# Performance work log

Measured on AMD Instinct MI355X. Metric: run time of the kernel, lower is better.

The kernel has to match this reference:

```python
import jax, jax.numpy as jnp
import numpy as np

EPS = 1e-5


def layer_norm(x, g, b):
    mu = jnp.mean(x, axis=-1, keepdims=True)
    var = jnp.mean((x - mu) ** 2, axis=-1, keepdims=True)
    return (x - mu) * jax.lax.rsqrt(var + EPS) * g + b


def rel_enc_shift(arr):
    # Transformer-XL shift trick: [b,n,l,m] -> shifted [b,n,l,m]
    b, n, l, m = arr.shape
    arr = jnp.concatenate([arr, jnp.zeros((b, n, l, 1), arr.dtype)], axis=-1)
    arr = arr.reshape(b, n, -1)
    arr = arr[:, :, l - 1:-1].reshape(b, n, l, m)
    return arr


def setup_inputs() -> dict:
    key = jax.random.key(0)
    B, S, M, D, H = 2, 1024, 1024, 1024, 16
    F = S + M
    ks = jax.random.split(key, 16)
    sc = 0.02
    inp = {
        "inputs": jax.random.normal(ks[0], (B, S, D), jnp.float32),
        "mem": jax.random.normal(ks[1], (B, M, D), jnp.float32),
        "rel_enc": jax.random.normal(ks[2], (F, D), jnp.float32),
        # causal mask with memory: query i may attend keys j <= i + M; 1 = masked
        "mask": (jnp.arange(F)[None, :] > (jnp.arange(S)[:, None] + M)).astype(jnp.float32)[None, None],
        "ln1_g": jnp.ones((D,), jnp.float32), "ln1_b": jnp.zeros((D,), jnp.float32),
        "wq": jax.random.normal(ks[3], (D, D), jnp.float32) * sc,
        "wke": jax.random.normal(ks[4], (D, D), jnp.float32) * sc,
        "wkr": jax.random.normal(ks[5], (D, D), jnp.float32) * sc,
        "wv": jax.random.normal(ks[6], (D, D), jnp.float32) * sc,
        "wf": jax.random.normal(ks[7], (D, D), jnp.float32) * sc,
        "u_param": jax.random.normal(ks[8], (1, 1, H, D // H), jnp.float32) * 0.05,
        "v_param": jax.random.normal(ks[9], (1, 1, H, D // H), jnp.float32) * 0.05,
        "ln2_g": jnp.ones((D,), jnp.float32), "ln2_b": jnp.zeros((D,), jnp.float32),
        "w1": jax.random.normal(ks[10], (D, D), jnp.float32) * sc,
        "b1": jnp.zeros((D,), jnp.float32),
        "w2": jax.random.normal(ks[11], (D, D), jnp.float32) * sc,
        "b2": jnp.zeros((D,), jnp.float32),
        "wg1": jax.random.normal(ks[12], (D, D), jnp.float32) * sc,
        "bg1": jnp.zeros((D,), jnp.float32),
        "wg2": jax.random.normal(ks[13], (D, D), jnp.float32) * sc,
        "bg2": jnp.zeros((D,), jnp.float32),
    }
    return inp


def _block(inputs, mem, mask, rel_enc, ln1_g, ln1_b, wq, wke, wkr, wv, wf,
           u_param, v_param, ln2_g, ln2_b, w1, b1, w2, b2, wg1, bg1, wg2, bg2):
    B, S, D = inputs.shape
    H = u_param.shape[2]
    dh = D // H
    x_tilde = jnp.concatenate([jax.lax.stop_gradient(mem), inputs], axis=1)
    F = x_tilde.shape[1]
    x_tilde = layer_norm(x_tilde, ln1_g, ln1_b)
    x = x_tilde[:, -S:, :]
    q = (x @ wq).reshape(B, S, H, dh)
    k = (x_tilde @ wke).reshape(B, F, H, dh)
    v = (x_tilde @ wv).reshape(B, F, H, dh)
    A_C = jnp.einsum('bsnd,bfnd->bnsf', q + u_param, k)
    Q = (rel_enc @ wkr).reshape(F, H, dh)
    B_D = rel_enc_shift(jnp.einsum('bsnd,fnd->bnsf', q + v_param, Q))
    score = (A_C + B_D) / jnp.sqrt(jnp.float32(D)) + mask * -1e10
    attn = jax.nn.softmax(score, axis=-1)
    attention_loss = jnp.mean(jnp.max(attn, axis=(-1, -2)))
    ao = jnp.einsum('bnsf,bfnd->bsnd', attn, v).reshape(B, S, D)
    rmha_out = jax.nn.gelu(ao @ wf, approximate=False)
    # gating 1 (output gating): x + sigmoid(Wx+b)*y
    g1 = inputs + jax.nn.sigmoid(inputs @ wg1 + bg1) * rmha_out
    h = layer_norm(g1, ln2_g, ln2_b)
    h = jax.nn.gelu(h @ w1 + b1, approximate=False)
    h = jax.nn.gelu(h @ w2 + b2, approximate=False)
    out = g1 + jax.nn.sigmoid(g1 @ wg2 + bg2) * h
    return out, attn, attention_loss


def reference(inputs, mem, mask, rel_enc, ln1_g, ln1_b, wq, wke, wkr, wv, wf,
              u_param, v_param, ln2_g, ln2_b, w1, b1, w2, b2, wg1, bg1, wg2, bg2):
    return _block(inputs, mem, mask, rel_enc, ln1_g, ln1_b, wq, wke, wkr, wv, wf,
                  u_param, v_param, ln2_g, ln2_b, w1, b1, w2, b2, wg1, bg1, wg2, bg2)
```

## Files before the change

### kernel.cpp

```cpp
#include <hip/hip_runtime.h>
#include <hip/hip_bf16.h>


typedef __attribute__((ext_vector_type(8))) short bf16x8;
typedef __attribute__((ext_vector_type(4))) float f32x4;

#define MFMA16(a, b, c) __builtin_amdgcn_mfma_f32_16x16x32_bf16((a), (b), (c), 0, 0, 0)

__device__ __forceinline__ unsigned short f2bf(float f) {
  union { __hip_bfloat16 h; unsigned short u; } cv;
  cv.h = __float2bfloat16(f);
  return cv.u;
}

__device__ __forceinline__ float bf2f(unsigned short u) {
  return __uint_as_float((unsigned)u << 16);
}

__device__ __forceinline__ float gelu_f(float x) {
  return 0.5f * x * (1.f + erff(x * 0.70710678118654752f));
}

struct W9 { const float* p[9]; };

__global__ __launch_bounds__(256) void k_init(
    const float* __restrict__ inputs, const float* __restrict__ mem,
    const float* __restrict__ rel_enc, const float* __restrict__ g1n,
    const float* __restrict__ b1n, W9 wp,
    unsigned short* __restrict__ xt, unsigned short* __restrict__ inb,
    unsigned short* __restrict__ reb, unsigned short* __restrict__ wT,
    float* __restrict__ amax) {
  int bid = blockIdx.x, tid = threadIdx.x;
  if (bid == 0 && tid < 32) amax[tid] = 0.f;
  if (bid < 4096) {
    __shared__ float red[8];
    int b = bid >> 11, fi = bid & 2047;
    const float* src = (fi < 1024)
        ? (mem + ((size_t)(b * 1024 + fi)) * 1024)
        : (inputs + ((size_t)(b * 1024 + fi - 1024)) * 1024);
    float4 x = ((const float4*)src)[tid];
    float s = x.x + x.y + x.z + x.w;
    float ss = x.x * x.x + x.y * x.y + x.z * x.z + x.w * x.w;
#pragma unroll
    for (int m = 32; m > 0; m >>= 1) {
      s += __shfl_down(s, m, 64);
      ss += __shfl_down(ss, m, 64);
    }
    int w = tid >> 6;
    if ((tid & 63) == 0) { red[w] = s; red[4 + w] = ss; }
    __syncthreads();
    s = red[0] + red[1] + red[2] + red[3];
    ss = red[4] + red[5] + red[6] + red[7];
    float mu = s * (1.f / 1024.f);
    float inv = rsqrtf(ss * (1.f / 1024.f) - mu * mu + 1e-5f);
    float4 g = ((const float4*)g1n)[tid];
    float4 bb = ((const float4*)b1n)[tid];
    ushort4 o;
    o.x = f2bf((x.x - mu) * inv * g.x + bb.x);
    o.y = f2bf((x.y - mu) * inv * g.y + bb.y);
    o.z = f2bf((x.z - mu) * inv * g.z + bb.z);
    o.w = f2bf((x.w - mu) * inv * g.w + bb.w);
    ((ushort4*)(xt + (size_t)bid * 1024))[tid] = o;
    if (fi >= 1024) {
      ushort4 r4;
      r4.x = f2bf(x.x); r4.y = f2bf(x.y); r4.z = f2bf(x.z); r4.w = f2bf(x.w);
      ((ushort4*)(inb + ((size_t)(b * 1024 + fi - 1024)) * 1024))[tid] = r4;
    }
  } else if (bid < 6144) {
    int r = bid - 4096;
    float4 x = ((const float4*)(rel_enc + (size_t)r * 1024))[tid];
    ushort4 o;
    o.x = f2bf(x.x); o.y = f2bf(x.y); o.z = f2bf(x.z); o.w = f2bf(x.w);
    ((ushort4*)(reb + (size_t)r * 1024))[tid] = o;
  } else {
    __shared__ float tl[64][65];
    int idx = bid - 6144;
    int m = idx >> 8;
    int t = idx & 255;
    int k0 = (t >> 4) << 6, n0 = (t & 15) << 6;
    const float* srcw = wp.p[m];
    int kr = tid >> 4, nc = (tid & 15) << 2;
#pragma unroll
    for (int i = 0; i < 4; ++i) {
      int krow = i * 16 + kr;
      float4 v = *(const float4*)(srcw + (size_t)(k0 + krow) * 1024 + n0 + nc);
      tl[nc + 0][krow] = v.x;
      tl[nc + 1][krow] = v.y;
      tl[nc + 2][krow] = v.z;
      tl[nc + 3][krow] = v.w;
    }
    __syncthreads();
    int n = tid >> 2, kc0 = (tid & 3) << 4;
    unsigned short* dst = wT + ((size_t)m << 20) + (size_t)(n0 + n) * 1024 + k0 + kc0;
#pragma unroll
    for (int q = 0; q < 4; ++q) {
      ushort4 o;
      o.x = f2bf(tl[n][kc0 + q * 4 + 0]);
      o.y = f2bf(tl[n][kc0 + q * 4 + 1]);
      o.z = f2bf(tl[n][kc0 + q * 4 + 2]);
      o.w = f2bf(tl[n][kc0 + q * 4 + 3]);
      *(ushort4*)(dst + q * 4) = o;
    }
  }
}

__global__ __launch_bounds__(256) void k_ln(
    const float* __restrict__ xin, const float* __restrict__ g1n,
    const float* __restrict__ b1n, unsigned short* __restrict__ outb) {
  __shared__ float red[8];
  int bid = blockIdx.x, tid = threadIdx.x;
  const float* src = xin + (size_t)bid * 1024;
  float4 x = ((const float4*)src)[tid];
  float s = x.x + x.y + x.z + x.w;
  float ss = x.x * x.x + x.y * x.y + x.z * x.z + x.w * x.w;
#pragma unroll
  for (int m = 32; m > 0; m >>= 1) {
    s += __shfl_down(s, m, 64);
    ss += __shfl_down(ss, m, 64);
  }
  int w = tid >> 6;
  if ((tid & 63) == 0) { red[w] = s; red[4 + w] = ss; }
  __syncthreads();
  s = red[0] + red[1] + red[2] + red[3];
  ss = red[4] + red[5] + red[6] + red[7];
  float mu = s * (1.f / 1024.f);
  float inv = rsqrtf(ss * (1.f / 1024.f) - mu * mu + 1e-5f);
  float4 g = ((const float4*)g1n)[tid];
  float4 bb = ((const float4*)b1n)[tid];
  ushort4 o;
  o.x = f2bf((x.x - mu) * inv * g.x + bb.x);
  o.y = f2bf((x.y - mu) * inv * g.y + bb.y);
  o.z = f2bf((x.z - mu) * inv * g.z + bb.z);
  o.w = f2bf((x.w - mu) * inv * g.w + bb.w);
  ((ushort4*)(outb + (size_t)bid * 1024))[tid] = o;
}

__device__ __forceinline__ int lds_u128(int r, int g) {
  return g * 128 + (r & ~7) + ((r ^ g) & 7);
}
template <int TM>
__device__ __forceinline__ int lds_uT(int r, int g) {
  return g * TM + (r & ~7) + ((r ^ g) & 7);
}

enum { EP_KV = 0, EP_QUV, EP_BF16, EP_GELU_F32, EP_GATE1,
       EP_GELU_B_BF16, EP_GELU_B_F32, EP_GATE2 };

template <int EP, int TM>
__global__ __launch_bounds__(256, 2) void k_gemm(
    const unsigned short* __restrict__ A, const unsigned short* __restrict__ Bw,
    int arow_add, int arow_mul,
    const float* __restrict__ bias, const float* __restrict__ auxA,
    const float* __restrict__ auxB, void* __restrict__ out0,
    void* __restrict__ out1) {
  constexpr int MI = TM / 16;
  constexpr int AU = TM / 32;
  __shared__ __align__(16) unsigned short As[2][TM * 64];
  __shared__ __align__(16) unsigned short Bs[2][128 * 64];
  int tid = threadIdx.x;
  int lane = tid & 63, wave = tid >> 6;
  int quad = lane >> 4, col = lane & 15;
  int bm = blockIdx.y, bn = blockIdx.x;
  f32x4 acc[MI][2] = {};
  int str = tid >> 3, stg = tid & 7;
  const unsigned short* aptr[AU];
  int au[AU];
  const unsigned short* bptr[4];
  int bu[4];
#pragma unroll
  for (int i = 0; i < AU; ++i) {
    int r = str + 32 * i;
    int gr = bm * TM + r;
    int ar = gr + arow_add + (gr >> 10) * arow_mul;
    aptr[i] = A + (size_t)ar * 1024 + stg * 8;
    au[i] = lds_uT<TM>(r, stg);
  }
#pragma unroll
  for (int i = 0; i < 4; ++i) {
    int r = str + 32 * i;
    bptr[i] = Bw + (size_t)(bn * 128 + r) * 1024 + stg * 8;
    bu[i] = lds_u128(r, stg);
  }
  uint4 av[AU], bv[4];
#pragma unroll
  for (int i = 0; i < AU; ++i) av[i] = *(const uint4*)(aptr[i]);
#pragma unroll
  for (int i = 0; i < 4; ++i) bv[i] = *(const uint4*)(bptr[i]);
#pragma unroll
  for (int i = 0; i < AU; ++i) ((uint4*)As[0])[au[i]] = av[i];
#pragma unroll
  for (int i = 0; i < 4; ++i) ((uint4*)Bs[0])[bu[i]] = bv[i];
  for (int kt = 0; kt < 16; ++kt) {
    __syncthreads();
    if (kt < 15) {
      int k0 = (kt + 1) * 64;
#pragma unroll
      for (int i = 0; i < AU; ++i) av[i] = *(const uint4*)(aptr[i] + k0);
#pragma unroll
      for (int i = 0; i < 4; ++i) bv[i] = *(const uint4*)(bptr[i] + k0);
    }
    int cur = kt & 1;
#pragma unroll
    for (int ks = 0; ks < 2; ++ks) {
      bf16x8 af[MI], bfr[2];
#pragma unroll
      for (int mi = 0; mi < MI; ++mi)
        af[mi] = ((const bf16x8*)As[cur])[lds_uT<TM>(mi * 16 + col, ks * 4 + quad)];
#pragma unroll
      for (int ni = 0; ni < 2; ++ni)
        bfr[ni] = ((const bf16x8*)Bs[cur])[lds_u128(wave * 32 + ni * 16 + col, ks * 4 + quad)];
#pragma unroll
      for (int mi = 0; mi < MI; ++mi)
#pragma unroll
        for (int ni = 0; ni < 2; ++ni)
          acc[mi][ni] = MFMA16(af[mi], bfr[ni], acc[mi][ni]);
    }
    if (kt < 15) {
      int nxt = cur ^ 1;
#pragma unroll
      for (int i = 0; i < AU; ++i) ((uint4*)As[nxt])[au[i]] = av[i];
#pragma unroll
      for (int i = 0; i < 4; ++i) ((uint4*)Bs[nxt])[bu[i]] = bv[i];
    }
  }
#pragma unroll
  for (int mi = 0; mi < MI; ++mi)
#pragma unroll
    for (int ni = 0; ni < 2; ++ni)
#pragma unroll
      for (int r = 0; r < 4; ++r) {
        int grow = bm * TM + mi * 16 + quad * 4 + r;
        int gcol = bn * 128 + wave * 32 + ni * 16 + col;
        float v = acc[mi][ni][r];
        size_t idx = (size_t)grow * 1024 + gcol;
        if constexpr (EP == EP_KV) {
          if (gcol < 1024) {
            ((unsigned short*)out0)[(size_t)grow * 1024 + gcol] = f2bf(v);
          } else {
            ((unsigned short*)out1)[(size_t)grow * 1024 + gcol - 1024] = f2bf(v);
          }
        } else if constexpr (EP == EP_QUV) {
          ((unsigned short*)out0)[idx] = f2bf(v + auxA[gcol]);
          ((unsigned short*)out1)[idx] = f2bf(v + auxB[gcol]);
        } else if constexpr (EP == EP_BF16) {
          ((unsigned short*)out0)[idx] = f2bf(v);
        } else if constexpr (EP == EP_GELU_F32) {
          ((float*)out0)[idx] = gelu_f(v);
        } else if constexpr (EP == EP_GATE1) {
          float a = v + bias[gcol];
          float sg = 1.f / (1.f + __expf(-a));
          float g1 = auxA[idx] + sg * auxB[idx];
          ((float*)out0)[idx] = g1;
          ((unsigned short*)out1)[idx] = f2bf(g1);
        } else if constexpr (EP == EP_GELU_B_BF16) {
          ((unsigned short*)out0)[idx] = f2bf(gelu_f(v + bias[gcol]));
        } else if constexpr (EP == EP_GELU_B_F32) {
          ((float*)out0)[idx] = gelu_f(v + bias[gcol]);
        } else {
          float a = v + bias[gcol];
          float sg = 1.f / (1.f + __expf(-a));
          ((float*)out0)[idx] = auxA[idx] + sg * auxB[idx];
        }
      }
}

__global__ __launch_bounds__(256) void k_tr(
    const unsigned short* __restrict__ v, unsigned short* __restrict__ vT) {
  __shared__ unsigned short tl[64][72];
  int bh = blockIdx.x, ft = blockIdx.y;
  int b = bh >> 4, h = bh & 15;
  int f0 = ft * 64;
  int tid = threadIdx.x;
  int fr = tid >> 2, c0 = (tid & 3) * 16;
  *(uint4*)&tl[fr][c0] =
      *(const uint4*)(v + ((size_t)(b * 2048 + f0 + fr)) * 1024 + h * 64 + c0);
  __syncthreads();
  int dr = tid >> 2, fc = (tid & 3) * 16;
  unsigned short* dst =
      vT + (((size_t)(b * 16 + h) * 64 + dr)) * 2048 + f0 + fc;
#pragma unroll
  for (int q = 0; q < 4; ++q) {
    ushort4 o;
    o.x = tl[fc + q * 4 + 0][dr];
    o.y = tl[fc + q * 4 + 1][dr];
    o.z = tl[fc + q * 4 + 2][dr];
    o.w = tl[fc + q * 4 + 3][dr];
    *(ushort4*)(dst + q * 4) = o;
  }
}

__global__ __launch_bounds__(256, 2) void k_att(
    const unsigned short* __restrict__ qu, const unsigned short* __restrict__ qv,
    const unsigned short* __restrict__ kk, const unsigned short* __restrict__ vT,
    const unsigned short* __restrict__ Qr,
    float* __restrict__ attn, unsigned short* __restrict__ ao,
    float* __restrict__ amax) {
  __shared__ __align__(16) unsigned short Pb[16][2056];
  __shared__ __align__(16) float Ol[2][1024];
  __shared__ float Sl[4][16];
  __shared__ float Rinv[16];
  int tid = threadIdx.x, lane = tid & 63, wave = tid >> 6;
  int quad = lane >> 4, col = lane & 15;
  int bh = blockIdx.x, rt = blockIdx.y;
  int b = bh >> 4, h = bh & 15;
  int ri = rt * 16;

  bf16x8 quf[2], qvf[2];
  {
    const unsigned short* p0 = qu + ((size_t)(b * 1024 + ri + col)) * 1024 + h * 64 + quad * 8;
    quf[0] = *(const bf16x8*)p0;
    quf[1] = *(const bf16x8*)(p0 + 32);
    const unsigned short* p1 = qv + ((size_t)(b * 1024 + ri + col)) * 1024 + h * 64 + quad * 8;
    qvf[0] = *(const bf16x8*)p1;
    qvf[1] = *(const bf16x8*)(p1 + 32);
  }

  const unsigned short* qrbase = Qr + h * 64 + quad * 8;
  auto r_load = [&](int cbase, bf16x8& b0, bf16x8& b1) {
    int cr = cbase + col;
    cr = cr < 0 ? 0 : (cr > 2047 ? 2047 : cr);
    const unsigned short* p = qrbase + (size_t)cr * 1024;
    b0 = *(const bf16x8*)p;
    b1 = *(const bf16x8*)(p + 32);
  };
  auto r_mm = [&](bf16x8 b0, bf16x8 b1) -> f32x4 {
    f32x4 z = {0.f, 0.f, 0.f, 0.f};
    z = MFMA16(qvf[0], b0, z);
    z = MFMA16(qvf[1], b1, z);
    return z;
  };

  const unsigned short* kbase = kk + ((size_t)(b * 2048)) * 1024 + h * 64 + quad * 8;
  const unsigned short* vbase = vT + ((size_t)((b * 16 + h) * 64)) * 2048;

  f32x4 o4[4] = {};
  f32x4 srow = {0.f, 0.f, 0.f, 0.f};
  f32x4 pm = {0.f, 0.f, 0.f, 0.f};
  int jmax = ri + 15 + 1024;
  int NA = (jmax >> 5) + 1;
  int myN = (NA - wave + 3) >> 2;

  auto load_chunk = [&](int j0, int cw, bf16x8* rr, bf16x8* kr, bf16x8* vr) {
    r_load(cw, rr[0], rr[1]);
    r_load(cw + 16, rr[2], rr[3]);
    r_load(cw + 32, rr[4], rr[5]);
    const unsigned short* kp0 = kbase + (size_t)(j0 + col) * 1024;
    const unsigned short* kp1 = kbase + (size_t)(j0 + 16 + col) * 1024;
    kr[0] = *(const bf16x8*)kp0;
    kr[1] = *(const bf16x8*)(kp0 + 32);
    kr[2] = *(const bf16x8*)kp1;
    kr[3] = *(const bf16x8*)(kp1 + 32);
    int fb = j0 + quad * 8;
#pragma unroll
    for (int ni = 0; ni < 4; ++ni)
      vr[ni] = *(const bf16x8*)(vbase + (size_t)(ni * 16 + col) * 2048 + fb);
  };

  auto compute_chunk = [&](int j0, bf16x8* rr, bf16x8* kr, bf16x8* vr) {
    f32x4 R0 = r_mm(rr[0], rr[1]);
    f32x4 R1 = r_mm(rr[2], rr[3]);
    f32x4 R2 = r_mm(rr[4], rr[5]);
    f32x4 ac0 = {0.f, 0.f, 0.f, 0.f};
    ac0 = MFMA16(quf[0], kr[0], ac0);
    ac0 = MFMA16(quf[1], kr[1], ac0);
    f32x4 ac1 = {0.f, 0.f, 0.f, 0.f};
    ac1 = MFMA16(quf[0], kr[2], ac1);
    ac1 = MFMA16(quf[1], kr[3], ac1);
#pragma unroll
    for (int r = 0; r < 4; ++r) {
      int w = 15 + col - quad * 4 - r;
      int src = quad * 16 + (w & 15);
      float bd0 = __shfl(R0[r], src, 64);
      float bd1 = __shfl(R1[r], src, 64);
      float bd = (w < 16) ? bd0 : bd1;
      float sc = (ac0[r] + bd) * 0.03125f;
      int masked = (j0 + col) > (ri + quad * 4 + r + 1024);
      float p = masked ? 0.f : __expf(sc);
      srow[r] += p;
      pm[r] = fmaxf(pm[r], p);
      Pb[quad * 4 + r][j0 + col] = f2bf(p);
    }
#pragma unroll
    for (int r = 0; r < 4; ++r) {
      int w = 15 + col - quad * 4 - r;
      int src = quad * 16 + (w & 15);
      float bd0 = __shfl(R1[r], src, 64);
      float bd1 = __shfl(R2[r], src, 64);
      float bd = (w < 16) ? bd0 : bd1;
      float sc = (ac1[r] + bd) * 0.03125f;
      int masked = (j0 + 16 + col) > (ri + quad * 4 + r + 1024);
      float p = masked ? 0.f : __expf(sc);
      srow[r] += p;
      pm[r] = fmaxf(pm[r], p);
      Pb[quad * 4 + r][j0 + 16 + col] = f2bf(p);
    }
    asm volatile("s_waitcnt lgkmcnt(0)" ::: "memory");
    bf16x8 pf = *(const bf16x8*)&Pb[col][j0 + quad * 8];
#pragma unroll
    for (int ni = 0; ni < 4; ++ni) o4[ni] = MFMA16(pf, vr[ni], o4[ni]);
  };

  {
    bf16x8 Ar[6], Ak[4], Av[4], Br[6], Bk[4], Bv[4];
    int j0 = wave << 5;
    int cw = 1008 - ri + j0;
    load_chunk(j0, cw, Ar, Ak, Av);
    int i = 0;
    while (true) {
      if (i + 1 < myN) load_chunk(j0 + 128, cw + 128, Br, Bk, Bv);
      compute_chunk(j0, Ar, Ak, Av);
      ++i; j0 += 128; cw += 128;
      if (i >= myN) break;
      if (i + 1 < myN) load_chunk(j0 + 128, cw + 128, Ar, Ak, Av);
      compute_chunk(j0, Br, Bk, Bv);
      ++i; j0 += 128; cw += 128;
      if (i >= myN) break;
    }
  }

#pragma unroll
  for (int r = 0; r < 4; ++r) {
    float v = srow[r], m = pm[r];
    v += __shfl_xor(v, 1, 64);  m = fmaxf(m, __shfl_xor(m, 1, 64));
    v += __shfl_xor(v, 2, 64);  m = fmaxf(m, __shfl_xor(m, 2, 64));
    v += __shfl_xor(v, 4, 64);  m = fmaxf(m, __shfl_xor(m, 4, 64));
    v += __shfl_xor(v, 8, 64);  m = fmaxf(m, __shfl_xor(m, 8, 64));
    srow[r] = v; pm[r] = m;
  }
  if (col == 0) {
#pragma unroll
    for (int r = 0; r < 4; ++r) Sl[wave][quad * 4 + r] = srow[r];
  }
  if (wave >= 2) {
#pragma unroll
    for (int ni = 0; ni < 4; ++ni)
#pragma unroll
      for (int r = 0; r < 4; ++r)
        Ol[wave - 2][(quad * 4 + r) * 64 + ni * 16 + col] = o4[ni][r];
  }
  __syncthreads();
  if (tid < 16) {
    float rv = 1.f / (Sl[0][tid] + Sl[1][tid] + Sl[2][tid] + Sl[3][tid]);
    Rinv[tid] = rv;
  }
  if (wave < 2) {
#pragma unroll
    for (int ni = 0; ni < 4; ++ni)
#pragma unroll
      for (int r = 0; r < 4; ++r) {
        int ix = (quad * 4 + r) * 64 + ni * 16 + col;
        o4[ni][r] += Ol[wave][ix];
        if (wave == 1) Ol[1][ix] = o4[ni][r];
      }
  }
  __syncthreads();
  if (wave == 0) {
#pragma unroll
    for (int ni = 0; ni < 4; ++ni)
#pragma unroll
      for (int r = 0; r < 4; ++r) {
        int ix = (quad * 4 + r) * 64 + ni * 16 + col;
        o4[ni][r] += Ol[1][ix];
        Ol[0][ix] = o4[ni][r];
      }
  }
  __syncthreads();
  {
    int row = tid >> 4, d0 = (tid & 15) << 2;
    float4 ov = *(const float4*)&Ol[0][row * 64 + d0];
    float rv = Rinv[row];
    ushort4 o;
    o.x = f2bf(ov.x * rv); o.y = f2bf(ov.y * rv);
    o.z = f2bf(ov.z * rv); o.w = f2bf(ov.w * rv);
    *(ushort4*)(ao + ((size_t)(b * 1024 + ri + row)) * 1024 + h * 64 + d0) = o;
  }
  float pmax = 0.f;
#pragma unroll
  for (int r = 0; r < 4; ++r) pmax = fmaxf(pmax, pm[r] * Rinv[quad * 4 + r]);
  pmax = fmaxf(pmax, __shfl_xor(pmax, 16, 64));
  pmax = fmaxf(pmax, __shfl_xor(pmax, 32, 64));
  if (lane == 0) atomicMax((int*)(amax + bh), __float_as_int(pmax));

  {
    float* abase = attn + ((size_t)bh * 1024 + ri) * 2048;
#pragma unroll 4
    for (int it = 0; it < 32; ++it) {
      int idx = it * 256 + tid;
      int row = idx >> 9;
      int j = (idx & 511) << 2;
      float rv = Rinv[row];
      int lim = ri + row + 1024;
      ushort4 p4 = *(const ushort4*)&Pb[row][j];
      float4 o;
      o.x = (j + 0 <= lim) ? bf2f(p4.x) * rv : 0.f;
      o.y = (j + 1 <= lim) ? bf2f(p4.y) * rv : 0.f;
      o.z = (j + 2 <= lim) ? bf2f(p4.z) * rv : 0.f;
      o.w = (j + 3 <= lim) ? bf2f(p4.w) * rv : 0.f;
      *(float4*)(abase + (size_t)row * 2048 + j) = o;
    }
  }
}

__global__ void k_loss(const float* __restrict__ amax, float* __restrict__ out) {
  int l = threadIdx.x;
  float v = (l < 32) ? amax[l] : 0.f;
  v += __shfl_xor(v, 1, 64);
  v += __shfl_xor(v, 2, 64);
  v += __shfl_xor(v, 4, 64);
  v += __shfl_xor(v, 8, 64);
  v += __shfl_xor(v, 16, 64);
  v += __shfl_xor(v, 32, 64);
  if (l == 0) out[0] = v * (1.f / 32.f);
}

extern "C" void kernel_launch(void* const* d_in, const int* in_sizes, int n_in,
                              void* d_out, int out_size, void* d_ws, size_t ws_size,
                              hipStream_t stream) {
  (void)in_sizes; (void)n_in; (void)out_size; (void)ws_size;
  const float* inputs = (const float*)d_in[0];
  const float* mem    = (const float*)d_in[1];
  const float* rel    = (const float*)d_in[2];
  const float* ln1g   = (const float*)d_in[4];
  const float* ln1b   = (const float*)d_in[5];
  const float* wq     = (const float*)d_in[6];
  const float* wke    = (const float*)d_in[7];
  const float* wkr    = (const float*)d_in[8];
  const float* wv     = (const float*)d_in[9];
  const float* wf     = (const float*)d_in[10];
  const float* up     = (const float*)d_in[11];
  const float* vp     = (const float*)d_in[12];
  const float* ln2g   = (const float*)d_in[13];
  const float* ln2b   = (const float*)d_in[14];
  const float* w1     = (const float*)d_in[15];
  const float* b1     = (const float*)d_in[16];
  const float* w2     = (const float*)d_in[17];
  const float* b2     = (const float*)d_in[18];
  const float* wg1    = (const float*)d_in[19];
  const float* bg1    = (const float*)d_in[20];
  const float* wg2    = (const float*)d_in[21];
  const float* bg2    = (const float*)d_in[22];

  char* ws = (char*)d_ws;
  unsigned short* wT  = (unsigned short*)(ws);
  unsigned short* xt  = (unsigned short*)(ws + 18874368);
  unsigned short* inb = (unsigned short*)(ws + 27262976);
  unsigned short* reb = (unsigned short*)(ws + 31457280);
  unsigned short* kb  = (unsigned short*)(ws + 35651584);
  unsigned short* vTb = (unsigned short*)(ws + 44040192);
  unsigned short* qub = (unsigned short*)(ws + 52428800);
  unsigned short* qvb = (unsigned short*)(ws + 56623104);
  unsigned short* Qrb = (unsigned short*)(ws + 60817408);
  float* amax         = (float*)(ws + 65011712);
  unsigned short* vb = qub;
  float* rmha = (float*)xt;
  unsigned short* aob = reb;
  float* g1f = (float*)kb;
  float* h2f = (float*)vTb;
  unsigned short* g1b = qub;
  unsigned short* h0b = qvb;
  unsigned short* h1b = Qrb;

  float* outp  = (float*)d_out;
  float* attnp = outp + 2097152;
  float* lossp = outp + 69206016;

  W9 wp;
  wp.p[0] = wq;  wp.p[1] = wke; wp.p[2] = wv;  wp.p[3] = wkr; wp.p[4] = wf;
  wp.p[5] = w1;  wp.p[6] = w2;  wp.p[7] = wg1; wp.p[8] = wg2;

  k_init<<<8448, 256, 0, stream>>>(inputs, mem, rel, ln1g, ln1b, wp,
                                   xt, inb, reb, wT, amax);
  k_gemm<EP_KV, 64><<<dim3(16, 64), 256, 0, stream>>>(
      xt, wT + (1u << 20), 0, 0, nullptr, nullptr, nullptr, kb, vb);
  k_tr<<<dim3(32, 32), 256, 0, stream>>>(vb, vTb);
  k_gemm<EP_QUV, 32><<<dim3(8, 64), 256, 0, stream>>>(
      xt, wT, 1024, 1024, nullptr, up, vp, qub, qvb);
  k_gemm<EP_BF16, 32><<<dim3(8, 64), 256, 0, stream>>>(
      reb, wT + 3u * (1u << 20), 0, 0, nullptr, nullptr, nullptr, Qrb, nullptr);
  k_att<<<dim3(32, 64), 256, 0, stream>>>(qub, qvb, kb, vTb, Qrb,
                                          attnp, aob, amax);
  k_gemm<EP_GELU_F32, 32><<<dim3(8, 64), 256, 0, stream>>>(
      aob, wT + 4u * (1u << 20), 0, 0, nullptr, nullptr, nullptr, rmha, nullptr);
  k_gemm<EP_GATE1, 32><<<dim3(8, 64), 256, 0, stream>>>(
      inb, wT + 7u * (1u << 20), 0, 0, bg1, inputs, rmha, g1f, g1b);
  k_ln<<<2048, 256, 0, stream>>>(g1f, ln2g, ln2b, h0b);
  k_gemm<EP_GELU_B_BF16, 32><<<dim3(8, 64), 256, 0, stream>>>(
      h0b, wT + 5u * (1u << 20), 0, 0, b1, nullptr, nullptr, h1b, nullptr);
  k_gemm<EP_GELU_B_F32, 32><<<dim3(8, 64), 256, 0, stream>>>(
      h1b, wT + 6u * (1u << 20), 0, 0, b2, nullptr, nullptr, h2f, nullptr);
  k_gemm<EP_GATE2, 32><<<dim3(8, 64), 256, 0, stream>>>(
      g1b, wT + 8u * (1u << 20), 0, 0, bg2, g1f, h2f, outp, nullptr);
  k_loss<<<1, 64, 0, stream>>>(amax, lossp);
}
```

Baseline: 709.0 us.

## Double attention waves per block, raise GEMM occupancy, use nontemporal attn stores

The attention kernel now runs 8 waves per block instead of 4. Key chunks are strided across 8 waves and the partial outputs are combined through an extra tree-reduction stage in shared memory. GEMM launch bounds ask for more resident blocks per CU, and the large fp32 attention-matrix write uses nontemporal stores to avoid polluting the cache. The aims are more latency hiding in attention and in the GEMMs, and cheaper streaming output writes. The costs are register pressure from the tighter launch bounds and extra barriers in the reduction.

```diff
diff --git a/kernel.cpp b/kernel.cpp
--- a/kernel.cpp
+++ b/kernel.cpp
@@ -147,7 +147,7 @@
        EP_GELU_B_BF16, EP_GELU_B_F32, EP_GATE2 };
 
 template <int EP, int TM>
-__global__ __launch_bounds__(256, 2) void k_gemm(
+__global__ __launch_bounds__(256, TM == 32 ? 4 : 3) void k_gemm(
     const unsigned short* __restrict__ A, const unsigned short* __restrict__ Bw,
     int arow_add, int arow_mul,
     const float* __restrict__ bias, const float* __restrict__ auxA,
@@ -289,7 +289,7 @@
   }
 }
 
-__global__ __launch_bounds__(256, 2) void k_att(
+__global__ __launch_bounds__(512, 4) void k_att(
     const unsigned short* __restrict__ qu, const unsigned short* __restrict__ qv,
     const unsigned short* __restrict__ kk, const unsigned short* __restrict__ vT,
     const unsigned short* __restrict__ Qr,
@@ -297,7 +297,7 @@
     float* __restrict__ amax) {
   __shared__ __align__(16) unsigned short Pb[16][2056];
   __shared__ __align__(16) float Ol[2][1024];
-  __shared__ float Sl[4][16];
+  __shared__ float Sl[8][16];
   __shared__ float Rinv[16];
   int tid = threadIdx.x, lane = tid & 63, wave = tid >> 6;
   int quad = lane >> 4, col = lane & 15;
@@ -338,7 +338,7 @@
   f32x4 pm = {0.f, 0.f, 0.f, 0.f};
   int jmax = ri + 15 + 1024;
   int NA = (jmax >> 5) + 1;
-  int myN = (NA - wave + 3) >> 2;
+  int myN = (NA - wave + 7) >> 3;
 
   auto load_chunk = [&](int j0, int cw, bf16x8* rr, bf16x8* kr, bf16x8* vr) {
     r_load(cw, rr[0], rr[1]);
@@ -407,13 +407,13 @@
     load_chunk(j0, cw, Ar, Ak, Av);
     int i = 0;
     while (true) {
-      if (i + 1 < myN) load_chunk(j0 + 128, cw + 128, Br, Bk, Bv);
+      if (i + 1 < myN) load_chunk(j0 + 256, cw + 256, Br, Bk, Bv);
       compute_chunk(j0, Ar, Ak, Av);
-      ++i; j0 += 128; cw += 128;
+      ++i; j0 += 256; cw += 256;
       if (i >= myN) break;
-      if (i + 1 < myN) load_chunk(j0 + 128, cw + 128, Ar, Ak, Av);
+      if (i + 1 < myN) load_chunk(j0 + 256, cw + 256, Ar, Ak, Av);
       compute_chunk(j0, Br, Bk, Bv);
-      ++i; j0 += 128; cw += 128;
+      ++i; j0 += 256; cw += 256;
       if (i >= myN) break;
     }
   }
@@ -431,18 +431,41 @@
 #pragma unroll
     for (int r = 0; r < 4; ++r) Sl[wave][quad * 4 + r] = srow[r];
   }
-  if (wave >= 2) {
+  if (wave >= 6) {
 #pragma unroll
     for (int ni = 0; ni < 4; ++ni)
 #pragma unroll
       for (int r = 0; r < 4; ++r)
-        Ol[wave - 2][(quad * 4 + r) * 64 + ni * 16 + col] = o4[ni][r];
+        Ol[wave - 6][(quad * 4 + r) * 64 + ni * 16 + col] = o4[ni][r];
   }
   __syncthreads();
   if (tid < 16) {
-    float rv = 1.f / (Sl[0][tid] + Sl[1][tid] + Sl[2][tid] + Sl[3][tid]);
+    float rv = 1.f / (Sl[0][tid] + Sl[1][tid] + Sl[2][tid] + Sl[3][tid] +
+                      Sl[4][tid] + Sl[5][tid] + Sl[6][tid] + Sl[7][tid]);
     Rinv[tid] = rv;
   }
+  if (wave == 4 || wave == 5) {
+#pragma unroll
+    for (int ni = 0; ni < 4; ++ni)
+#pragma unroll
+      for (int r = 0; r < 4; ++r) {
+        int ix = (quad * 4 + r) * 64 + ni * 16 + col;
+        o4[ni][r] += Ol[wave - 4][ix];
+        Ol[wave - 4][ix] = o4[ni][r];
+      }
+  }
+  __syncthreads();
+  if (wave == 2 || wave == 3) {
+#pragma unroll
+    for (int ni = 0; ni < 4; ++ni)
+#pragma unroll
+      for (int r = 0; r < 4; ++r) {
+        int ix = (quad * 4 + r) * 64 + ni * 16 + col;
+        o4[ni][r] += Ol[wave - 2][ix];
+        Ol[wave - 2][ix] = o4[ni][r];
+      }
+  }
+  __syncthreads();
   if (wave < 2) {
 #pragma unroll
     for (int ni = 0; ni < 4; ++ni)
@@ -465,7 +488,7 @@
       }
   }
   __syncthreads();
-  {
+  if (tid < 256) {
     int row = tid >> 4, d0 = (tid & 15) << 2;
     float4 ov = *(const float4*)&Ol[0][row * 64 + d0];
     float rv = Rinv[row];
@@ -484,19 +507,19 @@
   {
     float* abase = attn + ((size_t)bh * 1024 + ri) * 2048;
 #pragma unroll 4
-    for (int it = 0; it < 32; ++it) {
-      int idx = it * 256 + tid;
+    for (int it = 0; it < 16; ++it) {
+      int idx = it * 512 + tid;
       int row = idx >> 9;
       int j = (idx & 511) << 2;
       float rv = Rinv[row];
       int lim = ri + row + 1024;
       ushort4 p4 = *(const ushort4*)&Pb[row][j];
-      float4 o;
-      o.x = (j + 0 <= lim) ? bf2f(p4.x) * rv : 0.f;
-      o.y = (j + 1 <= lim) ? bf2f(p4.y) * rv : 0.f;
-      o.z = (j + 2 <= lim) ? bf2f(p4.z) * rv : 0.f;
-      o.w = (j + 3 <= lim) ? bf2f(p4.w) * rv : 0.f;
-      *(float4*)(abase + (size_t)row * 2048 + j) = o;
+      f32x4 o;
+      o[0] = (j + 0 <= lim) ? bf2f(p4.x) * rv : 0.f;
+      o[1] = (j + 1 <= lim) ? bf2f(p4.y) * rv : 0.f;
+      o[2] = (j + 2 <= lim) ? bf2f(p4.z) * rv : 0.f;
+      o[3] = (j + 3 <= lim) ? bf2f(p4.w) * rv : 0.f;
+      __builtin_nontemporal_store(o, (f32x4*)(abase + (size_t)row * 2048 + j));
     }
   }
 }
@@ -577,7 +600,7 @@
       xt, wT, 1024, 1024, nullptr, up, vp, qub, qvb);
   k_gemm<EP_BF16, 32><<<dim3(8, 64), 256, 0, stream>>>(
       reb, wT + 3u * (1u << 20), 0, 0, nullptr, nullptr, nullptr, Qrb, nullptr);
-  k_att<<<dim3(32, 64), 256, 0, stream>>>(qub, qvb, kb, vTb, Qrb,
+  k_att<<<dim3(32, 64), 512, 0, stream>>>(qub, qvb, kb, vTb, Qrb,
                                           attnp, aob, amax);
   k_gemm<EP_GELU_F32, 32><<<dim3(8, 64), 256, 0, stream>>>(
       aob, wT + 4u * (1u << 20), 0, 0, nullptr, nullptr, nullptr, rmha, nullptr);
```

Result: slower. 882.2 us (+24.4%).

## Store K and Qr head-major so attention loads are contiguous per head

Applied to the files above, without the earlier changes.

The K projection and relative-position Qr GEMM epilogues now write head-major layouts ([b,h,f,64] and [h,f,64]), and the attention kernel indexes them with a 64-element row stride instead of 1024. Each head's key and position rows become contiguous, which is meant to improve cache-line use and locality of the per-chunk fragment loads in attention. GEMM launch bounds are raised to 3–4 blocks per SM, and the attention kernel drops its min-blocks hint, which changes register allocation and occupancy. The GEMM epilogue stores become more scattered, and the occupancy change may cause register spills.

```diff
diff --git a/kernel.cpp b/kernel.cpp
--- a/kernel.cpp
+++ b/kernel.cpp
@@ -143,11 +143,11 @@
   return g * TM + (r & ~7) + ((r ^ g) & 7);
 }
 
-enum { EP_KV = 0, EP_QUV, EP_BF16, EP_GELU_F32, EP_GATE1,
+enum { EP_KV = 0, EP_QUV, EP_QR, EP_GELU_F32, EP_GATE1,
        EP_GELU_B_BF16, EP_GELU_B_F32, EP_GATE2 };
 
 template <int EP, int TM>
-__global__ __launch_bounds__(256, 2) void k_gemm(
+__global__ __launch_bounds__(256, TM == 32 ? 4 : 3) void k_gemm(
     const unsigned short* __restrict__ A, const unsigned short* __restrict__ Bw,
     int arow_add, int arow_mul,
     const float* __restrict__ bias, const float* __restrict__ auxA,
@@ -235,15 +235,18 @@
         size_t idx = (size_t)grow * 1024 + gcol;
         if constexpr (EP == EP_KV) {
           if (gcol < 1024) {
-            ((unsigned short*)out0)[(size_t)grow * 1024 + gcol] = f2bf(v);
+            size_t ki = (((size_t)(grow >> 11) * 16 + (gcol >> 6)) * 2048 +
+                         (grow & 2047)) * 64 + (gcol & 63);
+            ((unsigned short*)out0)[ki] = f2bf(v);
           } else {
             ((unsigned short*)out1)[(size_t)grow * 1024 + gcol - 1024] = f2bf(v);
           }
         } else if constexpr (EP == EP_QUV) {
           ((unsigned short*)out0)[idx] = f2bf(v + auxA[gcol]);
           ((unsigned short*)out1)[idx] = f2bf(v + auxB[gcol]);
-        } else if constexpr (EP == EP_BF16) {
-          ((unsigned short*)out0)[idx] = f2bf(v);
+        } else if constexpr (EP == EP_QR) {
+          size_t qi = ((size_t)(gcol >> 6) * 2048 + grow) * 64 + (gcol & 63);
+          ((unsigned short*)out0)[qi] = f2bf(v);
         } else if constexpr (EP == EP_GELU_F32) {
           ((float*)out0)[idx] = gelu_f(v);
         } else if constexpr (EP == EP_GATE1) {
@@ -289,7 +292,7 @@
   }
 }
 
-__global__ __launch_bounds__(256, 2) void k_att(
+__global__ __launch_bounds__(256) void k_att(
     const unsigned short* __restrict__ qu, const unsigned short* __restrict__ qv,
     const unsigned short* __restrict__ kk, const unsigned short* __restrict__ vT,
     const unsigned short* __restrict__ Qr,
@@ -315,11 +318,11 @@
     qvf[1] = *(const bf16x8*)(p1 + 32);
   }
 
-  const unsigned short* qrbase = Qr + h * 64 + quad * 8;
+  const unsigned short* qrbase = Qr + (size_t)h * 2048 * 64 + quad * 8;
   auto r_load = [&](int cbase, bf16x8& b0, bf16x8& b1) {
     int cr = cbase + col;
     cr = cr < 0 ? 0 : (cr > 2047 ? 2047 : cr);
-    const unsigned short* p = qrbase + (size_t)cr * 1024;
+    const unsigned short* p = qrbase + (size_t)cr * 64;
     b0 = *(const bf16x8*)p;
     b1 = *(const bf16x8*)(p + 32);
   };
@@ -330,7 +333,7 @@
     return z;
   };
 
-  const unsigned short* kbase = kk + ((size_t)(b * 2048)) * 1024 + h * 64 + quad * 8;
+  const unsigned short* kbase = kk + ((size_t)(b * 16 + h)) * 2048 * 64 + quad * 8;
   const unsigned short* vbase = vT + ((size_t)((b * 16 + h) * 64)) * 2048;
 
   f32x4 o4[4] = {};
@@ -344,8 +347,8 @@
     r_load(cw, rr[0], rr[1]);
     r_load(cw + 16, rr[2], rr[3]);
     r_load(cw + 32, rr[4], rr[5]);
-    const unsigned short* kp0 = kbase + (size_t)(j0 + col) * 1024;
-    const unsigned short* kp1 = kbase + (size_t)(j0 + 16 + col) * 1024;
+    const unsigned short* kp0 = kbase + (size_t)(j0 + col) * 64;
+    const unsigned short* kp1 = kbase + (size_t)(j0 + 16 + col) * 64;
     kr[0] = *(const bf16x8*)kp0;
     kr[1] = *(const bf16x8*)(kp0 + 32);
     kr[2] = *(const bf16x8*)kp1;
@@ -491,12 +494,12 @@
       float rv = Rinv[row];
       int lim = ri + row + 1024;
       ushort4 p4 = *(const ushort4*)&Pb[row][j];
-      float4 o;
-      o.x = (j + 0 <= lim) ? bf2f(p4.x) * rv : 0.f;
-      o.y = (j + 1 <= lim) ? bf2f(p4.y) * rv : 0.f;
-      o.z = (j + 2 <= lim) ? bf2f(p4.z) * rv : 0.f;
-      o.w = (j + 3 <= lim) ? bf2f(p4.w) * rv : 0.f;
-      *(float4*)(abase + (size_t)row * 2048 + j) = o;
+      f32x4 o;
+      o[0] = (j + 0 <= lim) ? bf2f(p4.x) * rv : 0.f;
+      o[1] = (j + 1 <= lim) ? bf2f(p4.y) * rv : 0.f;
+      o[2] = (j + 2 <= lim) ? bf2f(p4.z) * rv : 0.f;
+      o[3] = (j + 3 <= lim) ? bf2f(p4.w) * rv : 0.f;
+      *(f32x4*)(abase + (size_t)row * 2048 + j) = o;
     }
   }
 }
@@ -575,7 +578,7 @@
   k_tr<<<dim3(32, 32), 256, 0, stream>>>(vb, vTb);
   k_gemm<EP_QUV, 32><<<dim3(8, 64), 256, 0, stream>>>(
       xt, wT, 1024, 1024, nullptr, up, vp, qub, qvb);
-  k_gemm<EP_BF16, 32><<<dim3(8, 64), 256, 0, stream>>>(
+  k_gemm<EP_QR, 32><<<dim3(8, 64), 256, 0, stream>>>(
       reb, wT + 3u * (1u << 20), 0, 0, nullptr, nullptr, nullptr, Qrb, nullptr);
   k_att<<<dim3(32, 64), 256, 0, stream>>>(qub, qvb, kb, vTb, Qrb,
                                           attnp, aob, amax);
```

New measurement: 710.9 us. Within noise of the previous version (+0.3%).
